# Kernel optimization log

Hardware: AMD Instinct MI355X
Metric: run time of the kernel (lower is better)

Reference implementation:

```python
import jax, jax.numpy as jnp
import numpy as np

EMB = 2048
NH = 16
HD = EMB // NH  # 128

def setup_inputs() -> dict:
    key = jax.random.key(0)
    kx, kw1, kw2 = jax.random.split(key, 3)
    T = 4096
    x = jax.random.normal(kx, (T, EMB), dtype=jnp.float32)
    lim_in = 1.0 / np.sqrt(EMB)
    # input_proj: Linear(EMB, 3*EMB, use_bias=False), weight shape (out, in)
    W_in = jax.random.uniform(kw1, (3 * EMB, EMB), minval=-lim_in, maxval=lim_in, dtype=jnp.float32)
    W_out = jax.random.uniform(kw2, (EMB, EMB), minval=-lim_in, maxval=lim_in, dtype=jnp.float32)
    return {"x": x, "W_in": W_in, "W_out": W_out}

def reference(x, W_in, W_out):
    T = x.shape[0]
    norm = 1.0 / np.sqrt(HD)
    qkv = x @ W_in.T                         # [T, 3E]
    Q, K, V = jnp.split(qkv, 3, axis=-1)     # each [T, E]
    Q = Q.reshape(T, NH, HD).transpose(1, 0, 2)  # [nh, T, hd]
    K = K.reshape(T, NH, HD).transpose(1, 0, 2)
    V = V.reshape(T, NH, HD).transpose(1, 0, 2)
    A = jnp.einsum('htd,hsd->hts', Q, K) * norm  # [nh, T, T]
    mask = jnp.tri(T, dtype=bool)                # causal: keep lower triangle
    A = jnp.where(mask, A, -jnp.inf)
    P = jax.nn.softmax(A, axis=-1)
    y = jnp.einsum('hts,hsd->htd', P, V)         # [nh, T, hd]
    y = y.transpose(1, 0, 2).reshape(T, EMB)     # concat heads
    return y @ W_out.T
```

## Files before the change

### kernel.cpp

```cpp
#include <hip/hip_runtime.h>
#include <hip/hip_bf16.h>
#include <cstddef>


typedef __attribute__((ext_vector_type(8))) short short8;
typedef __attribute__((ext_vector_type(4))) float f32x4;

#define MFMA16(a, b, c) __builtin_amdgcn_mfma_f32_16x16x32_bf16((a), (b), (c), 0, 0, 0)

#define GLOAD_LDS16(gptr, lptr)                                                          \
  __builtin_amdgcn_global_load_lds((const __attribute__((address_space(1))) void*)(gptr), \
                                   (__attribute__((address_space(3))) void*)(lptr), 16, 0, 0)

#define PSWZ(q) ((((q) & 7) ^ ((q) >> 3)) << 3)

__device__ __forceinline__ short f2bf(float f) {
  __hip_bfloat16 h = __float2bfloat16(f);
  return *reinterpret_cast<short*>(&h);
}

__device__ __forceinline__ void storeC(float* p, float v) { *p = v; }
__device__ __forceinline__ void storeC(short* p, float v) { *p = f2bf(v); }

__global__ void cvt_bf16(const float* __restrict__ in, short* __restrict__ out,
                         long n, float scale, long scaleN) {
  long i = ((long)blockIdx.x * 256 + threadIdx.x) * 8;
  if (i >= n) return;
  float s = (i < scaleN) ? scale : 1.0f;
  f32x4 a = *(const f32x4*)(in + i);
  f32x4 b = *(const f32x4*)(in + i + 4);
  short8 o;
  o[0] = f2bf(a[0] * s); o[1] = f2bf(a[1] * s); o[2] = f2bf(a[2] * s); o[3] = f2bf(a[3] * s);
  o[4] = f2bf(b[0] * s); o[5] = f2bf(b[1] * s); o[6] = f2bf(b[2] * s); o[7] = f2bf(b[3] * s);
  *(short8*)(out + i) = o;
}

template <typename CT>
__global__ __launch_bounds__(256, 2)
void gemm_bt(const short* __restrict__ A, const short* __restrict__ B,
             CT* __restrict__ C, int M, int N, int K) {
  __shared__ short As[128 * 32];
  __shared__ short Bs[128 * 32];
  const int tid = threadIdx.x;
  const int wave = tid >> 6, lane = tid & 63;
  const int g = lane >> 4, fr = lane & 15;
  const int wr = (wave >> 1) * 64, wc = (wave & 1) * 64;
  const int bm = blockIdx.y * 128, bn = blockIdx.x * 128;

  f32x4 acc[4][4] = {};

  for (int k0 = 0; k0 < K; k0 += 32) {
    __syncthreads();
#pragma unroll
    for (int i = 0; i < 2; ++i) {
      int Ci = i * 256 + tid;
      int row = Ci >> 2, c = Ci & 3;
      int sc = c ^ (row & 3);
      GLOAD_LDS16(A + (size_t)(bm + row) * K + k0 + sc * 8, As + Ci * 8);
      GLOAD_LDS16(B + (size_t)(bn + row) * K + k0 + sc * 8, Bs + Ci * 8);
    }
    __syncthreads();

    short8 af[4], bfr[4];
#pragma unroll
    for (int m = 0; m < 4; ++m) {
      int row = wr + m * 16 + fr;
      int off = (g * 8) ^ ((row & 3) * 8);
      af[m] = *(const short8*)(As + row * 32 + off);
    }
#pragma unroll
    for (int n = 0; n < 4; ++n) {
      int row = wc + n * 16 + fr;
      int off = (g * 8) ^ ((row & 3) * 8);
      bfr[n] = *(const short8*)(Bs + row * 32 + off);
    }
#pragma unroll
    for (int m = 0; m < 4; ++m)
#pragma unroll
      for (int n = 0; n < 4; ++n)
        acc[m][n] = MFMA16(af[m], bfr[n], acc[m][n]);
  }

#pragma unroll
  for (int m = 0; m < 4; ++m) {
#pragma unroll
    for (int r = 0; r < 4; ++r) {
      size_t row = (size_t)(bm + wr + m * 16 + g * 4 + r);
      CT* cp = C + row * N + bn + wc + fr;
#pragma unroll
      for (int n = 0; n < 4; ++n)
        storeC(cp + n * 16, acc[m][n][r]);
    }
  }
}

__global__ __launch_bounds__(256, 4)
void vtrans(const short* __restrict__ qkv, short* __restrict__ vtg) {
  __shared__ short L[128 * 64];
  const int tid = threadIdx.x;
  const int tb = blockIdx.x * 64;
  const int h = blockIdx.y;
#pragma unroll
  for (int i = 0; i < 4; ++i) {
    int Ci = i * 256 + tid, tok = Ci >> 4, c = Ci & 15, f0 = c * 8;
    short8 v = *(const short8*)(qkv + (size_t)(tb + tok) * 6144 + 4096 + h * 128 + f0);
#pragma unroll
    for (int j = 0; j < 8; ++j) {
      int f = f0 + j;
      L[f * 64 + (tok ^ ((((f & 7) ^ ((f >> 3) & 7)) << 3)))] = v[j];
    }
  }
  __syncthreads();
  const int f = tid >> 1, half = (tid & 1) * 32;
  const int s_in = ((f & 7) ^ ((f >> 3) & 7)) << 3;
  const int s_out = (f & 7) << 3;
#pragma unroll
  for (int j2 = 0; j2 < 4; ++j2) {
    int t0 = half + j2 * 8;
    short8 v = *(const short8*)(&L[f * 64 + (t0 ^ s_in)]);
    *(short8*)(vtg + (size_t)(h * 128 + f) * 4096 + tb + (t0 ^ s_out)) = v;
  }
}

__global__ __launch_bounds__(256, 2)
void attn_fwd(const short* __restrict__ qkv, const short* __restrict__ vtg,
              short* __restrict__ y) {
  __shared__ short Ks[2][64 * 128];
  __shared__ short Vt[2][128 * 64];
  __shared__ short Ps[4][32 * 64];
  const int tid = threadIdx.x;
  const int wave = tid >> 6, lane = tid & 63;
  const int g = lane >> 4, fr = lane & 15;

  const int wgid = blockIdx.x;
  const int slot = wgid >> 3;
  const int h = ((wgid & 7) << 1) | (slot >> 4);
  const int pair = slot & 15;

  short* Pw = Ps[wave];

  short8 onesf;
#pragma unroll
  for (int j = 0; j < 8; ++j) onesf[j] = (short)0x3F80;

#pragma unroll 1
  for (int phase = 0; phase < 2; ++phase) {
    const int xb = phase ? (31 - pair) : pair;
    const int qw = xb * 128 + wave * 32;
    const int ntiles = 2 * xb + 2;

    short8 qf[2][4];
#pragma unroll
    for (int mi = 0; mi < 2; ++mi) {
      const short* Qp = qkv + (size_t)(qw + mi * 16 + fr) * 6144 + h * 128;
#pragma unroll
      for (int kk = 0; kk < 4; ++kk)
        qf[mi][kk] = *(const short8*)(Qp + kk * 32 + g * 8);
    }
    f32x4 oacc[2][8] = {};
    f32x4 lacc[2] = {};

#pragma unroll
    for (int i = 0; i < 4; ++i) {
      int Ci = i * 256 + tid, key = Ci >> 4, c = Ci & 15, sc = c ^ (key & 7);
      GLOAD_LDS16(qkv + (size_t)key * 6144 + 2048 + h * 128 + sc * 8, &Ks[0][Ci * 8]);
    }
#pragma unroll
    for (int i = 0; i < 4; ++i) {
      int Ci = i * 256 + tid, feat = Ci >> 3, ko = (Ci & 7) * 8;
      GLOAD_LDS16(vtg + (size_t)(h * 128 + feat) * 4096 + ko, &Vt[0][Ci * 8]);
    }
    __syncthreads();

#pragma unroll 1
    for (int t = 0; t < ntiles; ++t) {
      const int kv0 = t * 64;
      const int cur = t & 1;

      if (t + 1 < ntiles) {
#pragma unroll
        for (int i = 0; i < 4; ++i) {
          int Ci = i * 256 + tid, key = Ci >> 4, c = Ci & 15, sc = c ^ (key & 7);
          GLOAD_LDS16(qkv + (size_t)(kv0 + 64 + key) * 6144 + 2048 + h * 128 + sc * 8,
                      &Ks[cur ^ 1][Ci * 8]);
        }
#pragma unroll
        for (int i = 0; i < 4; ++i) {
          int Ci = i * 256 + tid, feat = Ci >> 3, ko = (Ci & 7) * 8;
          GLOAD_LDS16(vtg + (size_t)(h * 128 + feat) * 4096 + kv0 + 64 + ko,
                      &Vt[cur ^ 1][Ci * 8]);
        }
      }

      f32x4 s[2][4] = {};
      __builtin_amdgcn_s_setprio(1);
#pragma unroll
      for (int nf = 0; nf < 4; ++nf) {
        const int key = nf * 16 + fr;
#pragma unroll
        for (int kk = 0; kk < 4; ++kk) {
          int off = (kk * 32 + g * 8) ^ ((key & 7) * 8);
          short8 kfrag = *(const short8*)(&Ks[cur][key * 128 + off]);
          s[0][nf] = MFMA16(qf[0][kk], kfrag, s[0][nf]);
          s[1][nf] = MFMA16(qf[1][kk], kfrag, s[1][nf]);
        }
      }
      __builtin_amdgcn_s_setprio(0);

      if (t >= ntiles - 2) {
#pragma unroll
        for (int mi = 0; mi < 2; ++mi)
#pragma unroll
          for (int nf = 0; nf < 4; ++nf) {
            const int keyg = kv0 + nf * 16 + fr;
#pragma unroll
            for (int r = 0; r < 4; ++r) {
              const int q2 = mi * 16 + g * 4 + r;
              float p = (keyg <= qw + q2) ? __builtin_amdgcn_exp2f(s[mi][nf][r]) : 0.f;
              Pw[q2 * 64 + ((nf * 16 + fr) ^ PSWZ(q2))] = f2bf(p);
            }
          }
      } else {
#pragma unroll
        for (int mi = 0; mi < 2; ++mi)
#pragma unroll
          for (int nf = 0; nf < 4; ++nf)
#pragma unroll
            for (int r = 0; r < 4; ++r) {
              const int q2 = mi * 16 + g * 4 + r;
              Pw[q2 * 64 + ((nf * 16 + fr) ^ PSWZ(q2))] =
                  f2bf(__builtin_amdgcn_exp2f(s[mi][nf][r]));
            }
      }

      __builtin_amdgcn_s_setprio(1);
#pragma unroll
      for (int kk = 0; kk < 2; ++kk) {
        const int rb = kk * 32 + g * 8;
        short8 pf0 = *(const short8*)(&Pw[fr * 64 + (rb ^ PSWZ(fr))]);
        short8 pf1 = *(const short8*)(&Pw[(16 + fr) * 64 + (rb ^ PSWZ(16 + fr))]);
        lacc[0] = MFMA16(pf0, onesf, lacc[0]);
        lacc[1] = MFMA16(pf1, onesf, lacc[1]);
#pragma unroll
        for (int nf = 0; nf < 8; ++nf) {
          int f = nf * 16 + fr;
          short8 vf = *(const short8*)(&Vt[cur][f * 64 + (rb ^ ((f & 7) * 8))]);
          oacc[0][nf] = MFMA16(pf0, vf, oacc[0][nf]);
          oacc[1][nf] = MFMA16(pf1, vf, oacc[1][nf]);
        }
      }
      __builtin_amdgcn_s_setprio(0);

      __syncthreads();
    }

#pragma unroll
    for (int mi = 0; mi < 2; ++mi)
#pragma unroll
      for (int r = 0; r < 4; ++r) {
        float inv = 1.0f / lacc[mi][r];
        size_t row = (size_t)(qw + mi * 16 + g * 4 + r);
#pragma unroll
        for (int nf = 0; nf < 8; ++nf)
          y[row * 2048 + h * 128 + nf * 16 + fr] = f2bf(oacc[mi][nf][r] * inv);
      }
  }
}

extern "C" void kernel_launch(void* const* d_in, const int* in_sizes, int n_in,
                              void* d_out, int out_size, void* d_ws, size_t ws_size,
                              hipStream_t stream) {
  const float* x    = (const float*)d_in[0];
  const float* Win  = (const float*)d_in[1];
  const float* Wout = (const float*)d_in[2];
  float* out = (float*)d_out;

  char* ws = (char*)d_ws;
  short* xb    = (short*)(ws);
  short* yb    = (short*)(ws);
  short* Winb  = (short*)(ws + 16777216);
  short* vtg   = (short*)(ws + 16777216);
  short* Woutb = (short*)(ws + 41943040);
  short* qkv   = (short*)(ws + 50331648);

  const float qscale = 0.08838834764831845f * 1.4426950408889634f;

  cvt_bf16<<<4096, 256, 0, stream>>>(x, xb, 8388608L, 1.0f, 0L);
  cvt_bf16<<<6144, 256, 0, stream>>>(Win, Winb, 12582912L, qscale, 4194304L);
  cvt_bf16<<<2048, 256, 0, stream>>>(Wout, Woutb, 4194304L, 1.0f, 0L);

  gemm_bt<short><<<dim3(48, 32), 256, 0, stream>>>(xb, Winb, qkv, 4096, 6144, 2048);

  vtrans<<<dim3(64, 16), 256, 0, stream>>>(qkv, vtg);

  attn_fwd<<<256, 256, 0, stream>>>(qkv, vtg, yb);

  gemm_bt<float><<<dim3(16, 32), 256, 0, stream>>>(yb, Woutb, out, 4096, 2048, 2048);
}
```

Measured before the change: 341.1 us.

## Halve attention query tile to 64 rows, doubling grid; widen GEMM K-step to 64

The attention kernel now gives each wave 16 query rows instead of 32, so a workgroup covers 64 queries and the grid doubles to 512 workgroups. That spreads the causal work over more CUs and cuts per-wave registers and the P buffer in LDS, at the cost of loading each K/V tile twice as often per query. Separately, the GEMM loads 64-wide K slices with an 8-way swizzle, halving the number of barrier iterations, and raises the launch-bounds occupancy hint to 4. The larger LDS footprint (32 KB per GEMM block) and extra register pressure may prevent the 4-block occupancy target from being reached.

```diff
diff --git a/kernel.cpp b/kernel.cpp
--- a/kernel.cpp
+++ b/kernel.cpp
@@ -36,11 +36,11 @@
 }
 
 template <typename CT>
-__global__ __launch_bounds__(256, 2)
+__global__ __launch_bounds__(256, 4)
 void gemm_bt(const short* __restrict__ A, const short* __restrict__ B,
              CT* __restrict__ C, int M, int N, int K) {
-  __shared__ short As[128 * 32];
-  __shared__ short Bs[128 * 32];
+  __shared__ short As[128 * 64];
+  __shared__ short Bs[128 * 64];
   const int tid = threadIdx.x;
   const int wave = tid >> 6, lane = tid & 63;
   const int g = lane >> 4, fr = lane & 15;
@@ -49,36 +49,39 @@
 
   f32x4 acc[4][4] = {};
 
-  for (int k0 = 0; k0 < K; k0 += 32) {
+  for (int k0 = 0; k0 < K; k0 += 64) {
     __syncthreads();
 #pragma unroll
-    for (int i = 0; i < 2; ++i) {
+    for (int i = 0; i < 4; ++i) {
       int Ci = i * 256 + tid;
-      int row = Ci >> 2, c = Ci & 3;
-      int sc = c ^ (row & 3);
+      int row = Ci >> 3, c = Ci & 7;
+      int sc = c ^ (row & 7);
       GLOAD_LDS16(A + (size_t)(bm + row) * K + k0 + sc * 8, As + Ci * 8);
       GLOAD_LDS16(B + (size_t)(bn + row) * K + k0 + sc * 8, Bs + Ci * 8);
     }
     __syncthreads();
 
-    short8 af[4], bfr[4];
-#pragma unroll
-    for (int m = 0; m < 4; ++m) {
-      int row = wr + m * 16 + fr;
-      int off = (g * 8) ^ ((row & 3) * 8);
-      af[m] = *(const short8*)(As + row * 32 + off);
-    }
-#pragma unroll
-    for (int n = 0; n < 4; ++n) {
-      int row = wc + n * 16 + fr;
-      int off = (g * 8) ^ ((row & 3) * 8);
-      bfr[n] = *(const short8*)(Bs + row * 32 + off);
-    }
-#pragma unroll
-    for (int m = 0; m < 4; ++m)
-#pragma unroll
-      for (int n = 0; n < 4; ++n)
-        acc[m][n] = MFMA16(af[m], bfr[n], acc[m][n]);
+#pragma unroll
+    for (int kk = 0; kk < 2; ++kk) {
+      short8 af[4], bfr[4];
+#pragma unroll
+      for (int m = 0; m < 4; ++m) {
+        int row = wr + m * 16 + fr;
+        int off = (kk * 32 + g * 8) ^ ((row & 7) * 8);
+        af[m] = *(const short8*)(As + row * 64 + off);
+      }
+#pragma unroll
+      for (int n = 0; n < 4; ++n) {
+        int row = wc + n * 16 + fr;
+        int off = (kk * 32 + g * 8) ^ ((row & 7) * 8);
+        bfr[n] = *(const short8*)(Bs + row * 64 + off);
+      }
+#pragma unroll
+      for (int m = 0; m < 4; ++m)
+#pragma unroll
+        for (int n = 0; n < 4; ++n)
+          acc[m][n] = MFMA16(af[m], bfr[n], acc[m][n]);
+    }
   }
 
 #pragma unroll
@@ -127,15 +130,15 @@
               short* __restrict__ y) {
   __shared__ short Ks[2][64 * 128];
   __shared__ short Vt[2][128 * 64];
-  __shared__ short Ps[4][32 * 64];
+  __shared__ short Ps[4][16 * 64];
   const int tid = threadIdx.x;
   const int wave = tid >> 6, lane = tid & 63;
   const int g = lane >> 4, fr = lane & 15;
 
   const int wgid = blockIdx.x;
   const int slot = wgid >> 3;
-  const int h = ((wgid & 7) << 1) | (slot >> 4);
-  const int pair = slot & 15;
+  const int h = ((wgid & 7) << 1) | (slot >> 5);
+  const int pair = slot & 31;
 
   short* Pw = Ps[wave];
 
@@ -145,20 +148,19 @@
 
 #pragma unroll 1
   for (int phase = 0; phase < 2; ++phase) {
-    const int xb = phase ? (31 - pair) : pair;
-    const int qw = xb * 128 + wave * 32;
-    const int ntiles = 2 * xb + 2;
-
-    short8 qf[2][4];
-#pragma unroll
-    for (int mi = 0; mi < 2; ++mi) {
-      const short* Qp = qkv + (size_t)(qw + mi * 16 + fr) * 6144 + h * 128;
+    const int xb = phase ? (63 - pair) : pair;
+    const int qw = xb * 64 + wave * 16;
+    const int ntiles = xb + 1;
+
+    short8 qf[4];
+    {
+      const short* Qp = qkv + (size_t)(qw + fr) * 6144 + h * 128;
 #pragma unroll
       for (int kk = 0; kk < 4; ++kk)
-        qf[mi][kk] = *(const short8*)(Qp + kk * 32 + g * 8);
-    }
-    f32x4 oacc[2][8] = {};
-    f32x4 lacc[2] = {};
+        qf[kk] = *(const short8*)(Qp + kk * 32 + g * 8);
+    }
+    f32x4 oacc[8] = {};
+    f32x4 lacc = {};
 
 #pragma unroll
     for (int i = 0; i < 4; ++i) {
@@ -192,7 +194,7 @@
         }
       }
 
-      f32x4 s[2][4] = {};
+      f32x4 s[4] = {};
       __builtin_amdgcn_s_setprio(1);
 #pragma unroll
       for (int nf = 0; nf < 4; ++nf) {
@@ -201,52 +203,44 @@
         for (int kk = 0; kk < 4; ++kk) {
           int off = (kk * 32 + g * 8) ^ ((key & 7) * 8);
           short8 kfrag = *(const short8*)(&Ks[cur][key * 128 + off]);
-          s[0][nf] = MFMA16(qf[0][kk], kfrag, s[0][nf]);
-          s[1][nf] = MFMA16(qf[1][kk], kfrag, s[1][nf]);
+          s[nf] = MFMA16(qf[kk], kfrag, s[nf]);
         }
       }
       __builtin_amdgcn_s_setprio(0);
 
-      if (t >= ntiles - 2) {
-#pragma unroll
-        for (int mi = 0; mi < 2; ++mi)
-#pragma unroll
-          for (int nf = 0; nf < 4; ++nf) {
-            const int keyg = kv0 + nf * 16 + fr;
-#pragma unroll
-            for (int r = 0; r < 4; ++r) {
-              const int q2 = mi * 16 + g * 4 + r;
-              float p = (keyg <= qw + q2) ? __builtin_amdgcn_exp2f(s[mi][nf][r]) : 0.f;
-              Pw[q2 * 64 + ((nf * 16 + fr) ^ PSWZ(q2))] = f2bf(p);
-            }
+      if (t == ntiles - 1) {
+#pragma unroll
+        for (int nf = 0; nf < 4; ++nf) {
+          const int keyg = kv0 + nf * 16 + fr;
+#pragma unroll
+          for (int r = 0; r < 4; ++r) {
+            const int q = g * 4 + r;
+            float p = (keyg <= qw + q) ? __builtin_amdgcn_exp2f(s[nf][r]) : 0.f;
+            Pw[q * 64 + ((nf * 16 + fr) ^ PSWZ(q))] = f2bf(p);
           }
+        }
       } else {
 #pragma unroll
-        for (int mi = 0; mi < 2; ++mi)
-#pragma unroll
-          for (int nf = 0; nf < 4; ++nf)
-#pragma unroll
-            for (int r = 0; r < 4; ++r) {
-              const int q2 = mi * 16 + g * 4 + r;
-              Pw[q2 * 64 + ((nf * 16 + fr) ^ PSWZ(q2))] =
-                  f2bf(__builtin_amdgcn_exp2f(s[mi][nf][r]));
-            }
+        for (int nf = 0; nf < 4; ++nf)
+#pragma unroll
+          for (int r = 0; r < 4; ++r) {
+            const int q = g * 4 + r;
+            Pw[q * 64 + ((nf * 16 + fr) ^ PSWZ(q))] =
+                f2bf(__builtin_amdgcn_exp2f(s[nf][r]));
+          }
       }
 
       __builtin_amdgcn_s_setprio(1);
 #pragma unroll
       for (int kk = 0; kk < 2; ++kk) {
         const int rb = kk * 32 + g * 8;
-        short8 pf0 = *(const short8*)(&Pw[fr * 64 + (rb ^ PSWZ(fr))]);
-        short8 pf1 = *(const short8*)(&Pw[(16 + fr) * 64 + (rb ^ PSWZ(16 + fr))]);
-        lacc[0] = MFMA16(pf0, onesf, lacc[0]);
-        lacc[1] = MFMA16(pf1, onesf, lacc[1]);
+        short8 pf = *(const short8*)(&Pw[fr * 64 + (rb ^ PSWZ(fr))]);
+        lacc = MFMA16(pf, onesf, lacc);
 #pragma unroll
         for (int nf = 0; nf < 8; ++nf) {
           int f = nf * 16 + fr;
           short8 vf = *(const short8*)(&Vt[cur][f * 64 + (rb ^ ((f & 7) * 8))]);
-          oacc[0][nf] = MFMA16(pf0, vf, oacc[0][nf]);
-          oacc[1][nf] = MFMA16(pf1, vf, oacc[1][nf]);
+          oacc[nf] = MFMA16(pf, vf, oacc[nf]);
         }
       }
       __builtin_amdgcn_s_setprio(0);
@@ -255,15 +249,13 @@
     }
 
 #pragma unroll
-    for (int mi = 0; mi < 2; ++mi)
-#pragma unroll
-      for (int r = 0; r < 4; ++r) {
-        float inv = 1.0f / lacc[mi][r];
-        size_t row = (size_t)(qw + mi * 16 + g * 4 + r);
-#pragma unroll
-        for (int nf = 0; nf < 8; ++nf)
-          y[row * 2048 + h * 128 + nf * 16 + fr] = f2bf(oacc[mi][nf][r] * inv);
-      }
+    for (int r = 0; r < 4; ++r) {
+      float inv = 1.0f / lacc[r];
+      size_t row = (size_t)(qw + g * 4 + r);
+#pragma unroll
+      for (int nf = 0; nf < 8; ++nf)
+        y[row * 2048 + h * 128 + nf * 16 + fr] = f2bf(oacc[nf][r] * inv);
+    }
   }
 }
 
@@ -293,7 +285,7 @@
 
   vtrans<<<dim3(64, 16), 256, 0, stream>>>(qkv, vtg);
 
-  attn_fwd<<<256, 256, 0, stream>>>(qkv, vtg, yb);
+  attn_fwd<<<512, 256, 0, stream>>>(qkv, vtg, yb);
 
   gemm_bt<float><<<dim3(16, 32), 256, 0, stream>>>(yb, Woutb, out, 4096, 2048, 2048);
 }
```

New measurement: 292.2 us. 1.17x faster.
